# Optimization experiments

Measured on AMD Instinct MI355X. Metric: run time of the kernel, lower is better.

The kernel has to match this reference:

```python
import jax, jax.numpy as jnp
import numpy as np

N_QUBITS = 10
LAYERS = 4


def _ry(theta):
    c = jnp.cos(theta / 2).astype(jnp.complex64)
    s = jnp.sin(theta / 2).astype(jnp.complex64)
    return jnp.array([[c, -s], [s, c]], dtype=jnp.complex64)


def _rot(phi, theta, omega):
    # Rot = RZ(omega) RY(theta) RZ(phi)  (PennyLane convention)
    c = jnp.cos(theta / 2)
    s = jnp.sin(theta / 2)
    e_mm = jnp.exp(-0.5j * (phi + omega))
    e_pm = jnp.exp(0.5j * (phi - omega))
    e_mp = jnp.exp(-0.5j * (phi - omega))
    e_pp = jnp.exp(0.5j * (phi + omega))
    return jnp.array([[e_mm * c, -e_pm * s], [e_mp * s, e_pp * c]], dtype=jnp.complex64)


def _apply_1q(state, U, q):
    # state: (2,)*n complex; contract qubit axis q with 2x2 gate
    s = jnp.tensordot(U, state, axes=[[1], [q]])
    return jnp.moveaxis(s, 0, q)


def _apply_cnot(state, c, t):
    s = jnp.moveaxis(state, (c, t), (0, 1))
    s = jnp.stack([s[0], s[1, ::-1]], axis=0)
    return jnp.moveaxis(s, (0, 1), (c, t))


def _circuit(angles, weights):
    # angles: (n_qubits,) float32, weights: (layers, n_qubits, 3) float32
    n = N_QUBITS
    state = jnp.zeros((2 ** n,), dtype=jnp.complex64).at[0].set(1.0).reshape((2,) * n)
    for q in range(n):  # RY angle embedding
        state = _apply_1q(state, _ry(angles[q]), q)
    for l in range(LAYERS):  # strongly-entangling layers
        for q in range(n):
            state = _apply_1q(state, _rot(weights[l, q, 0], weights[l, q, 1], weights[l, q, 2]), q)
        for q in range(n):  # CNOT ring
            state = _apply_cnot(state, q, (q + 1) % n)
    probs = state.real ** 2 + state.imag ** 2  # (2,)*n
    zexp = []
    for q in range(n):
        p = probs.sum(axis=tuple(a for a in range(n) if a != q))
        zexp.append(p[0] - p[1])
    return jnp.stack(zexp)  # (n_qubits,)


def setup_inputs() -> dict:
    key = jax.random.key(0)
    ks = jax.random.split(key, 6)
    B, D = 8192, 784
    return {
        "x": jax.random.normal(ks[0], (B, D), dtype=jnp.float32),
        "Wp": jax.random.normal(ks[1], (N_QUBITS, D), dtype=jnp.float32) * (1.0 / np.sqrt(D)),
        "bp": jax.random.normal(ks[2], (N_QUBITS,), dtype=jnp.float32) * 0.01,
        "q_weights": jax.random.normal(ks[3], (LAYERS, N_QUBITS, 3), dtype=jnp.float32) * 0.01,
        "Wo": jax.random.normal(ks[4], (10, N_QUBITS), dtype=jnp.float32) * (1.0 / np.sqrt(N_QUBITS)),
        "bo": jax.random.normal(ks[5], (10,), dtype=jnp.float32) * 0.01,
    }


def reference(x, Wp, bp, q_weights, Wo, bo):
    # input projection + tanh
    h = jnp.tanh(x @ Wp.T + bp)  # (B, n_qubits)
    # batched quantum circuit (vmapped statevector simulation)
    q_out = jax.vmap(_circuit, in_axes=(0, None))(h, q_weights)  # (B, n_qubits)
    return q_out @ Wo.T + bo  # (B, 10) logits
```

## Files before the change

kernel.cpp:

```cpp
#include <hip/hip_runtime.h>

#define NQ      10
#define NLAYERS 4
#define D_IN    784
#define BLOCK   256


typedef __attribute__((ext_vector_type(2))) float f2;

__device__ __forceinline__ f2 cswapneg(f2 v) {
    f2 r; r.x = -v.y; r.y = v.x; return r;
}

template<int LB>
__device__ __forceinline__ float lane_xor(float v) {
    if constexpr (LB == 1) {
        return __int_as_float(__builtin_amdgcn_update_dpp(
            0, __float_as_int(v), 0xB1, 0xF, 0xF, false));
    } else if constexpr (LB == 2) {
        return __int_as_float(__builtin_amdgcn_update_dpp(
            0, __float_as_int(v), 0x4E, 0xF, 0xF, false));
    } else {
        return __shfl_xor(v, LB, 64);
    }
}

template<int LB>
__device__ __forceinline__ f2 lane_xor2(f2 v) {
    f2 r; r.x = lane_xor<LB>(v.x); r.y = lane_xor<LB>(v.y); return r;
}

template<int P>
__device__ __forceinline__ void rot_gate(f2 (&a)[16], int lane, float4 gA, float4 gB) {
    if constexpr (P >= 4) {
        const int lb = 1 << (P - 4);
        const bool hi = (lane & lb) != 0;
        const float gdx = hi ? gB.z : gA.x, gdy = hi ? gB.w : gA.y;
        const float gox = hi ? gB.x : gA.z, goy = hi ? gB.y : gA.w;
#pragma unroll
        for (int r = 0; r < 16; r++) {
            f2 oa = lane_xor2<lb>(a[r]);
            f2 va = a[r];
            a[r] = gdx * va + gdy * cswapneg(va) + gox * oa + goy * cswapneg(oa);
        }
    } else {
        const int m = 1 << P;
#pragma unroll
        for (int r = 0; r < 16; r++) {
            if (!(r & m)) {
                const int r1 = r | m;
                f2 A0 = a[r], A1 = a[r1];
                f2 ia0 = cswapneg(A0), ia1 = cswapneg(A1);
                a[r]  = gA.x * A0 + gA.y * ia0 + gA.z * A1 + gA.w * ia1;
                a[r1] = gB.x * A0 + gB.y * ia0 + gB.z * A1 + gB.w * ia1;
            }
        }
    }
}

__device__ __forceinline__ void rot9_fused(f2 (&a)[16], int lane, float4 gA, float4 gB) {
    const bool hi = (lane & 32) != 0;
    const float gdx = hi ? gB.z : gA.x, gdy = hi ? gB.w : gA.y;
    const float gox = hi ? gB.x : gA.z, goy = hi ? gB.y : gA.w;
#pragma unroll
    for (int r = 0; r < 16; r++) {
        f2 oa; oa.x = __shfl_xor(a[r].x, 32, 64); oa.y = __shfl_xor(a[r].y, 32, 64);
        f2 va = a[r];
        if (!(r & 1)) {
            a[r] = gdx * va + gdy * cswapneg(va) + gox * oa + goy * cswapneg(oa);
        } else {
            a[r] = gdx * oa + gdy * cswapneg(oa) + gox * va + goy * cswapneg(va);
        }
    }
}

template<int PC, int PT>
__device__ __forceinline__ void cnot_gate(f2 (&a)[16], int lane) {
    if constexpr (PC >= 4 && PT < 4) {
        const int mt = 1 << PT;
        const bool ctl = (lane & (1 << (PC - 4))) != 0;
#pragma unroll
        for (int r = 0; r < 16; r++) {
            if (!(r & mt)) {
                const int r1 = r | mt;
                f2 A0 = a[r], A1 = a[r1];
                f2 n0, n1;
                n0.x = ctl ? A1.x : A0.x;  n0.y = ctl ? A1.y : A0.y;
                n1.x = ctl ? A0.x : A1.x;  n1.y = ctl ? A0.y : A1.y;
                a[r] = n0; a[r1] = n1;
            }
        }
    } else if constexpr (PC < 4 && PT >= 4) {
        const int mc = 1 << PC, mt = 1 << (PT - 4);
#pragma unroll
        for (int r = 0; r < 16; r++) {
            if (r & mc) {
                a[r].x = __shfl_xor(a[r].x, mt, 64);
                a[r].y = __shfl_xor(a[r].y, mt, 64);
            }
        }
    } else {
        const int mc = 1 << PC, mt = 1 << PT;
#pragma unroll
        for (int r = 0; r < 16; r++) {
            if ((r & mc) && !(r & mt)) {
                const int r1 = r | mt;
                f2 t = a[r]; a[r] = a[r1]; a[r1] = t;
            }
        }
    }
}

__global__ __launch_bounds__(BLOCK)
__attribute__((amdgpu_waves_per_eu(8, 8)))
void qnet_kernel(
    const float* __restrict__ x,
    const float* __restrict__ Wp,
    const float* __restrict__ bp,
    const float* __restrict__ qw,
    const float* __restrict__ Wo,
    const float* __restrict__ bo,
    float* __restrict__ out, int B)
{
    __shared__ __align__(16) float gates[NLAYERS * NQ * 8];

    const int tid  = threadIdx.x;
    const int lane = tid & 63;
    const int s    = blockIdx.x * (BLOCK / 64) + (tid >> 6);

    if (tid < NLAYERS * NQ) {
        float phi = qw[tid * 3 + 0];
        float th  = qw[tid * 3 + 1];
        float om  = qw[tid * 3 + 2];
        float sth, cth; sincosf(0.5f * th, &sth, &cth);
        float sap, cap; sincosf(0.5f * (phi + om), &sap, &cap);
        float sam, cam; sincosf(0.5f * (phi - om), &sam, &cam);
        float* g = &gates[tid * 8];
        g[0] =  cap * cth;  g[1] = -sap * cth;
        g[2] = -cam * sth;  g[3] = -sam * sth;
        g[4] =  cam * sth;  g[5] = -sam * sth;
        g[6] =  cap * cth;  g[7] =  sap * cth;
    }
    __syncthreads();
    if (s >= B) return;

    float acc[NQ];
#pragma unroll
    for (int q = 0; q < NQ; q++) acc[q] = 0.f;
    const float* xr = x + (size_t)s * D_IN;
    for (int d = lane; d < D_IN; d += 64) {
        float xv = xr[d];
#pragma unroll
        for (int q = 0; q < NQ; q++) acc[q] += xv * Wp[q * D_IN + d];
    }
#pragma unroll
    for (int q = 0; q < NQ; q++) {
#pragma unroll
        for (int o = 1; o < 64; o <<= 1) acc[q] += __shfl_xor(acc[q], o, 64);
    }
    float myc = 1.f, mys = 0.f;
    if (lane < NQ) {
        float h = tanhf(acc[lane] + bp[lane]);
        sincosf(0.5f * h, &mys, &myc);
    }

    f2 a[16];
#pragma unroll
    for (int r = 0; r < 16; r++) { a[r].x = 0.f; a[r].y = 0.f; }
    if (lane == 0) a[0].x = 1.f;

    const int bidx = (lane ^ (lane >> 1)) << 2;

    {
        const float* gl = &gates[0];
#define FROTQ(Q) { \
        float c0  = __shfl(myc, Q, 64); \
        float ss0 = __shfl(mys, Q, 64); \
        float4 gA = *(const float4*)(gl + Q * 8); \
        float4 gB = *(const float4*)(gl + Q * 8 + 4); \
        float4 Am, Bm; \
        Am.x = gA.x * c0 + gA.z * ss0;  Am.y = gA.y * c0 + gA.w * ss0; \
        Am.z = gA.z * c0 - gA.x * ss0;  Am.w = gA.w * c0 - gA.y * ss0; \
        Bm.x = gB.x * c0 + gB.z * ss0;  Bm.y = gB.y * c0 + gB.w * ss0; \
        Bm.z = gB.z * c0 - gB.x * ss0;  Bm.w = gB.w * c0 - gB.y * ss0; \
        rot_gate<9 - Q>(a, lane, Am, Bm); }
        FROTQ(0) FROTQ(1) FROTQ(2) FROTQ(3) FROTQ(4)
        FROTQ(5) FROTQ(6) FROTQ(7) FROTQ(8) FROTQ(9)
#undef FROTQ
#pragma unroll
        for (int r = 0; r < 16; r++) {
            a[r].x = __int_as_float(__builtin_amdgcn_ds_bpermute(bidx, __float_as_int(a[r].x)));
            a[r].y = __int_as_float(__builtin_amdgcn_ds_bpermute(bidx, __float_as_int(a[r].y)));
        }
        cnot_gate<4, 3>(a, lane);
        cnot_gate<3, 2>(a, lane);
        cnot_gate<2, 1>(a, lane);
        cnot_gate<1, 0>(a, lane);
    }

    for (int l = 1; l < NLAYERS; l++) {
        const float* gl = &gates[l * NQ * 8];
        {   float4 gA = *(const float4*)(gl);
            float4 gB = *(const float4*)(gl + 4);
            rot9_fused(a, lane, gA, gB); }
#define ROTQ(Q) { float4 gA = *(const float4*)(gl + Q * 8); \
                  float4 gB = *(const float4*)(gl + Q * 8 + 4); \
                  rot_gate<9 - Q>(a, lane, gA, gB); }
        ROTQ(1) ROTQ(2) ROTQ(3) ROTQ(4)
        ROTQ(5) ROTQ(6) ROTQ(7) ROTQ(8) ROTQ(9)
#undef ROTQ
#pragma unroll
        for (int r = 0; r < 16; r++) {
            a[r].x = __int_as_float(__builtin_amdgcn_ds_bpermute(bidx, __float_as_int(a[r].x)));
            a[r].y = __int_as_float(__builtin_amdgcn_ds_bpermute(bidx, __float_as_int(a[r].y)));
        }
        cnot_gate<4, 3>(a, lane);
        cnot_gate<3, 2>(a, lane);
        cnot_gate<2, 1>(a, lane);
        cnot_gate<1, 0>(a, lane);
    }
    cnot_gate<0, 9>(a, lane);

    float S = 0.f, z3 = 0.f, z2 = 0.f, z1 = 0.f, z0 = 0.f;
#pragma unroll
    for (int r = 0; r < 16; r++) {
        float pa = a[r].x * a[r].x + a[r].y * a[r].y;
        S += pa;
        z3 += (r & 8) ? -pa : pa;
        z2 += (r & 4) ? -pa : pa;
        z1 += (r & 2) ? -pa : pa;
        z0 += (r & 1) ? -pa : pa;
    }
    float zq[NQ];
    zq[6] = z3; zq[7] = z2; zq[8] = z1; zq[9] = z0;
#pragma unroll
    for (int q = 0; q < 6; q++) {
        zq[q] = ((lane >> (5 - q)) & 1) ? -S : S;
    }
#pragma unroll
    for (int q = 0; q < NQ; q++) {
#pragma unroll
        for (int o = 1; o < 64; o <<= 1) {
            zq[q] += __shfl_xor(zq[q], o, 64);
        }
    }

    if (lane < NQ) {
        const float* wrow = Wo + lane * NQ;
        float o0 = bo[lane];
#pragma unroll
        for (int q = 0; q < NQ; q++) o0 += zq[q] * wrow[q];
        out[(size_t)s * NQ + lane] = o0;
    }
}

extern "C" void kernel_launch(void* const* d_in, const int* in_sizes, int n_in,
                              void* d_out, int out_size, void* d_ws, size_t ws_size,
                              hipStream_t stream) {
    const float* x  = (const float*)d_in[0];
    const float* Wp = (const float*)d_in[1];
    const float* bp = (const float*)d_in[2];
    const float* qw = (const float*)d_in[3];
    const float* Wo = (const float*)d_in[4];
    const float* bo = (const float*)d_in[5];
    float* out = (float*)d_out;

    const int B = in_sizes[0] / D_IN;
    const int spb = BLOCK / 64;
    const int blocks = (B + spb - 1) / spb;
    hipLaunchKernelGGL(qnet_kernel, dim3(blocks), dim3(BLOCK), 0, stream,
                       x, Wp, bp, qw, Wo, bo, out, B);
}
```

Baseline: 166.9 us.

## Use permlane swaps for cross-half rotations and vectorize the input projection

The rotations on the two highest lane-bit qubits (lane bits 32 and 16) now use permlane32/permlane16 swap instructions instead of bpermute-based shuffles. Each pair of registers is swapped across lane halves, the 2x2 gate is applied locally, and the pair is swapped back. The input projection now uses float4 loads of x and Wp with a tail step for the remaining elements. The waves-per-EU hint is relaxed from exactly 8 to a 4–8 range, giving the compiler more register room at some cost to occupancy.

```diff
diff --git a/kernel.cpp b/kernel.cpp
--- a/kernel.cpp
+++ b/kernel.cpp
@@ -30,6 +30,53 @@
     f2 r; r.x = lane_xor<LB>(v.x); r.y = lane_xor<LB>(v.y); return r;
 }
 
+template<int HALF>
+__device__ __forceinline__ void plswap(f2 &d, f2 &s) {
+    if constexpr (HALF == 32) {
+        auto rx = __builtin_amdgcn_permlane32_swap(__float_as_int(d.x), __float_as_int(s.x), false, false);
+        auto ry = __builtin_amdgcn_permlane32_swap(__float_as_int(d.y), __float_as_int(s.y), false, false);
+        d.x = __int_as_float(rx[0]); s.x = __int_as_float(rx[1]);
+        d.y = __int_as_float(ry[0]); s.y = __int_as_float(ry[1]);
+    } else {
+        auto rx = __builtin_amdgcn_permlane16_swap(__float_as_int(d.x), __float_as_int(s.x), false, false);
+        auto ry = __builtin_amdgcn_permlane16_swap(__float_as_int(d.y), __float_as_int(s.y), false, false);
+        d.x = __int_as_float(rx[0]); s.x = __int_as_float(rx[1]);
+        d.y = __int_as_float(ry[0]); s.y = __int_as_float(ry[1]);
+    }
+}
+
+template<int HALF>
+__device__ __forceinline__ void rot_gate_pl(f2 (&a)[16], float4 gA, float4 gB) {
+#pragma unroll
+    for (int r = 0; r < 16; r += 2) {
+        f2 u = a[r], v = a[r + 1];
+        plswap<HALF>(u, v);
+        f2 iu = cswapneg(u), iv = cswapneg(v);
+        f2 nu = gA.x * u + gA.y * iu + gA.z * v + gA.w * iv;
+        f2 nv = gB.x * u + gB.y * iu + gB.z * v + gB.w * iv;
+        plswap<HALF>(nu, nv);
+        a[r] = nu; a[r + 1] = nv;
+    }
+}
+
+__device__ __forceinline__ void rot9_fused_pl(f2 (&a)[16], int lane, float4 gA, float4 gB) {
+    const bool hi = (lane & 32) != 0;
+    const float cux = hi ? gA.z : gA.x, cuy = hi ? gA.w : gA.y;
+    const float cvx = hi ? gA.x : gA.z, cvy = hi ? gA.y : gA.w;
+    const float dux = hi ? gB.z : gB.x, duy = hi ? gB.w : gB.y;
+    const float dvx = hi ? gB.x : gB.z, dvy = hi ? gB.y : gB.w;
+#pragma unroll
+    for (int r = 0; r < 16; r += 2) {
+        f2 u = a[r], v = a[r + 1];
+        plswap<32>(u, v);
+        f2 iu = cswapneg(u), iv = cswapneg(v);
+        f2 nu = cux * u + cuy * iu + cvx * v + cvy * iv;
+        f2 nv = dux * u + duy * iu + dvx * v + dvy * iv;
+        plswap<32>(nu, nv);
+        a[r] = nu; a[r + 1] = nv;
+    }
+}
+
 template<int P>
 __device__ __forceinline__ void rot_gate(f2 (&a)[16], int lane, float4 gA, float4 gB) {
     if constexpr (P >= 4) {
@@ -54,22 +101,6 @@
                 a[r]  = gA.x * A0 + gA.y * ia0 + gA.z * A1 + gA.w * ia1;
                 a[r1] = gB.x * A0 + gB.y * ia0 + gB.z * A1 + gB.w * ia1;
             }
-        }
-    }
-}
-
-__device__ __forceinline__ void rot9_fused(f2 (&a)[16], int lane, float4 gA, float4 gB) {
-    const bool hi = (lane & 32) != 0;
-    const float gdx = hi ? gB.z : gA.x, gdy = hi ? gB.w : gA.y;
-    const float gox = hi ? gB.x : gA.z, goy = hi ? gB.y : gA.w;
-#pragma unroll
-    for (int r = 0; r < 16; r++) {
-        f2 oa; oa.x = __shfl_xor(a[r].x, 32, 64); oa.y = __shfl_xor(a[r].y, 32, 64);
-        f2 va = a[r];
-        if (!(r & 1)) {
-            a[r] = gdx * va + gdy * cswapneg(va) + gox * oa + goy * cswapneg(oa);
-        } else {
-            a[r] = gdx * oa + gdy * cswapneg(oa) + gox * va + goy * cswapneg(va);
         }
     }
 }
@@ -112,7 +143,7 @@
 }
 
 __global__ __launch_bounds__(BLOCK)
-__attribute__((amdgpu_waves_per_eu(8, 8)))
+__attribute__((amdgpu_waves_per_eu(4, 8)))
 void qnet_kernel(
     const float* __restrict__ x,
     const float* __restrict__ Wp,
@@ -148,10 +179,24 @@
 #pragma unroll
     for (int q = 0; q < NQ; q++) acc[q] = 0.f;
     const float* xr = x + (size_t)s * D_IN;
-    for (int d = lane; d < D_IN; d += 64) {
-        float xv = xr[d];
-#pragma unroll
-        for (int q = 0; q < NQ; q++) acc[q] += xv * Wp[q * D_IN + d];
+#pragma unroll
+    for (int it = 0; it < 3; it++) {
+        const int d = (it * 64 + lane) * 4;
+        float4 xv = *(const float4*)(xr + d);
+#pragma unroll
+        for (int q = 0; q < NQ; q++) {
+            float4 wv = *(const float4*)(Wp + q * D_IN + d);
+            acc[q] += xv.x * wv.x + xv.y * wv.y + xv.z * wv.z + xv.w * wv.w;
+        }
+    }
+    if (lane < 4) {
+        const int d = (192 + lane) * 4;
+        float4 xv = *(const float4*)(xr + d);
+#pragma unroll
+        for (int q = 0; q < NQ; q++) {
+            float4 wv = *(const float4*)(Wp + q * D_IN + d);
+            acc[q] += xv.x * wv.x + xv.y * wv.y + xv.z * wv.z + xv.w * wv.w;
+        }
     }
 #pragma unroll
     for (int q = 0; q < NQ; q++) {
@@ -173,7 +218,7 @@
 
     {
         const float* gl = &gates[0];
-#define FROTQ(Q) { \
+#define MKMAT(Q) \
         float c0  = __shfl(myc, Q, 64); \
         float ss0 = __shfl(mys, Q, 64); \
         float4 gA = *(const float4*)(gl + Q * 8); \
@@ -182,11 +227,18 @@
         Am.x = gA.x * c0 + gA.z * ss0;  Am.y = gA.y * c0 + gA.w * ss0; \
         Am.z = gA.z * c0 - gA.x * ss0;  Am.w = gA.w * c0 - gA.y * ss0; \
         Bm.x = gB.x * c0 + gB.z * ss0;  Bm.y = gB.y * c0 + gB.w * ss0; \
-        Bm.z = gB.z * c0 - gB.x * ss0;  Bm.w = gB.w * c0 - gB.y * ss0; \
-        rot_gate<9 - Q>(a, lane, Am, Bm); }
-        FROTQ(0) FROTQ(1) FROTQ(2) FROTQ(3) FROTQ(4)
-        FROTQ(5) FROTQ(6) FROTQ(7) FROTQ(8) FROTQ(9)
-#undef FROTQ
+        Bm.z = gB.z * c0 - gB.x * ss0;  Bm.w = gB.w * c0 - gB.y * ss0;
+        { MKMAT(0); rot_gate_pl<32>(a, Am, Bm); }
+        { MKMAT(1); rot_gate_pl<16>(a, Am, Bm); }
+        { MKMAT(2); rot_gate<7>(a, lane, Am, Bm); }
+        { MKMAT(3); rot_gate<6>(a, lane, Am, Bm); }
+        { MKMAT(4); rot_gate<5>(a, lane, Am, Bm); }
+        { MKMAT(5); rot_gate<4>(a, lane, Am, Bm); }
+        { MKMAT(6); rot_gate<3>(a, lane, Am, Bm); }
+        { MKMAT(7); rot_gate<2>(a, lane, Am, Bm); }
+        { MKMAT(8); rot_gate<1>(a, lane, Am, Bm); }
+        { MKMAT(9); rot_gate<0>(a, lane, Am, Bm); }
+#undef MKMAT
 #pragma unroll
         for (int r = 0; r < 16; r++) {
             a[r].x = __int_as_float(__builtin_amdgcn_ds_bpermute(bidx, __float_as_int(a[r].x)));
@@ -202,11 +254,14 @@
         const float* gl = &gates[l * NQ * 8];
         {   float4 gA = *(const float4*)(gl);
             float4 gB = *(const float4*)(gl + 4);
-            rot9_fused(a, lane, gA, gB); }
+            rot9_fused_pl(a, lane, gA, gB); }
+        {   float4 gA = *(const float4*)(gl + 8);
+            float4 gB = *(const float4*)(gl + 12);
+            rot_gate_pl<16>(a, gA, gB); }
 #define ROTQ(Q) { float4 gA = *(const float4*)(gl + Q * 8); \
                   float4 gB = *(const float4*)(gl + Q * 8 + 4); \
                   rot_gate<9 - Q>(a, lane, gA, gB); }
-        ROTQ(1) ROTQ(2) ROTQ(3) ROTQ(4)
+        ROTQ(2) ROTQ(3) ROTQ(4)
         ROTQ(5) ROTQ(6) ROTQ(7) ROTQ(8) ROTQ(9)
 #undef ROTQ
 #pragma unroll
```

Measured after the change: 162.0 us. -2.9%, faster.
